# Optimization experiments

Measured on AMD Instinct MI355X. Metric: run time of the kernel, lower is better.

## Reference

```python
import jax, jax.numpy as jnp
import numpy as np

B, T, D, H, O = 128, 1024, 256, 512, 128


def _uniform(key, shape, std):
    return jax.random.uniform(key, shape, jnp.float32, -std, std)


def setup_inputs() -> dict:
    key = jax.random.key(0)
    ks = jax.random.split(key, 12)
    std = 1.0 / np.sqrt(H)
    return {
        "x": jax.random.normal(ks[0], (B, T, D), jnp.float32),
        "EC_in": jax.random.normal(ks[1], (B, T, D), jnp.float32),
        "Wx": _uniform(ks[2], (4 * H, D), std),   # x2h weight
        "bx": _uniform(ks[3], (4 * H,), std),
        "Wh": _uniform(ks[4], (4 * H, H), std),   # h2h weight
        "bh": _uniform(ks[5], (4 * H,), std),
        "Wec": _uniform(ks[6], (H, D), std),      # EC weight (dead code in original)
        "bec": _uniform(ks[7], (H,), std),
        "Wfc": _uniform(ks[8], (O, H), std),      # final fc weight
        "bfc": _uniform(ks[9], (O,), std),
    }


def _lstm_forward(x, EC_in, Wx, bx, Wh, bh, Wec, bec, Wfc, bfc):
    # Precompute input projections for all timesteps: [B,T,4H] -> [T,B,4H]
    xg = jnp.einsum("btd,gd->tbg", x, Wx) + bx + bh
    # NOTE: original computes self.EC(EC_in) per step but never uses it (dead code).

    def step(carry, xg_t):
        h, c = carry
        gates = xg_t + h @ Wh.T  # [B, 4H]
        i, f, g, o = jnp.split(gates, 4, axis=1)
        i = jax.nn.sigmoid(i)
        f = jax.nn.sigmoid(f)
        g = jnp.tanh(g)
        o = jax.nn.sigmoid(o)
        c = c * f + i * g
        h = o * jnp.tanh(c)
        return (h, c), None

    h0 = jnp.zeros((x.shape[0], Wh.shape[1]), x.dtype)
    (hT, cT), _ = jax.lax.scan(step, (h0, h0), xg)
    out = hT @ Wfc.T + bfc
    return hT, out


def reference(x, EC_in, Wx, bx, Wh, bh, Wec, bec, Wfc, bfc):
    return _lstm_forward(x, EC_in, Wx, bx, Wh, bh, Wec, bec, Wfc, bfc)
```

## Files before the change

### kernel.cpp

```cpp
#include <hip/hip_runtime.h>

typedef __bf16 bf16;
typedef __bf16 bf16x4 __attribute__((ext_vector_type(4)));
typedef __bf16 bf16x8 __attribute__((ext_vector_type(8)));
typedef float f32x4 __attribute__((ext_vector_type(4)));
typedef unsigned int u32;
typedef unsigned long long u64;

#define T_STEPS 1024
#define BATCH 128
#define DIM 256
#define HID 512
#define NB 128
#define NGRP 8
#define GB 16
#define FLAGS_BYTES 16384

__device__ __forceinline__ f32x4 mfma_bf16(bf16x8 a, bf16x8 b, f32x4 c) {
  return __builtin_amdgcn_mfma_f32_16x16x32_bf16(a, b, c, 0, 0, 0);
}
__device__ __forceinline__ float fast_sigmoid(float v) {
  return __builtin_amdgcn_rcpf(1.f + __expf(-v));
}
__device__ __forceinline__ float fast_tanh(float v) {
  return 2.f * __builtin_amdgcn_rcpf(1.f + __expf(-2.f * v)) - 1.f;
}
__device__ __forceinline__ bf16x8 cvt8(const float* p) {
  float4 a = *(const float4*)p;
  float4 b = *(const float4*)(p + 4);
  bf16x8 r;
  r[0] = (bf16)a.x; r[1] = (bf16)a.y; r[2] = (bf16)a.z; r[3] = (bf16)a.w;
  r[4] = (bf16)b.x; r[5] = (bf16)b.y; r[6] = (bf16)b.z; r[7] = (bf16)b.w;
  return r;
}
__device__ __forceinline__ bf16x8 cvt8v(float4 a, float4 b) {
  bf16x8 r;
  r[0] = (bf16)a.x; r[1] = (bf16)a.y; r[2] = (bf16)a.z; r[3] = (bf16)a.w;
  r[4] = (bf16)b.x; r[5] = (bf16)b.y; r[6] = (bf16)b.z; r[7] = (bf16)b.w;
  return r;
}
__device__ __forceinline__ u32 pack_bf16x2(float a, float b) {
  unsigned short lo = __builtin_bit_cast(unsigned short, (bf16)a);
  unsigned short hi = __builtin_bit_cast(unsigned short, (bf16)b);
  return (u32)lo | ((u32)hi << 16);
}
__device__ __forceinline__ bf16x8 combine(u64 lo, u64 hi) {
  bf16x4 l4 = __builtin_bit_cast(bf16x4, lo);
  bf16x4 h4 = __builtin_bit_cast(bf16x4, hi);
  bf16x8 r;
  r[0] = l4[0]; r[1] = l4[1]; r[2] = l4[2]; r[3] = l4[3];
  r[4] = h4[0]; r[5] = h4[1]; r[6] = h4[2]; r[7] = h4[3];
  return r;
}
__device__ __forceinline__ u64 ld_agent(const u64* p) {
  return __hip_atomic_load(p, __ATOMIC_RELAXED, __HIP_MEMORY_SCOPE_AGENT);
}

__device__ __forceinline__ void wait_all128(const u32* flags, int lane, u32 target) {
  const u32* p0 = flags + (size_t)lane * 16;
  const u32* p1 = flags + (size_t)(64 + lane) * 16;
  u32 a = __hip_atomic_load(p0, __ATOMIC_RELAXED, __HIP_MEMORY_SCOPE_AGENT);
  u32 b = __hip_atomic_load(p1, __ATOMIC_RELAXED, __HIP_MEMORY_SCOPE_AGENT);
  while (!__all((a >= target) && (b >= target))) {
    __builtin_amdgcn_s_sleep(1);
    a = __hip_atomic_load(p0, __ATOMIC_RELAXED, __HIP_MEMORY_SCOPE_AGENT);
    b = __hip_atomic_load(p1, __ATOMIC_RELAXED, __HIP_MEMORY_SCOPE_AGENT);
  }
}

__global__ __launch_bounds__(256, 1) void lstm_persist(
    const float* __restrict__ x, const float* __restrict__ Wx,
    const float* __restrict__ bx, const float* __restrict__ Wh,
    const float* __restrict__ bh, const float* __restrict__ Wfc,
    const float* __restrict__ bfc, float* __restrict__ out,
    u32* flags, bf16* hbuf) {
  const int tid = threadIdx.x;
  const int bid = blockIdx.x;
  const int wave = tid >> 6;
  const int lane = tid & 63;
  const int n = lane & 15;
  const int quad = lane >> 4;
  const int sub = n & 3;
  const int bg = bid & 7;
  const int cg = bid >> 3;
  const int mbase = bg * GB;

  __shared__ bf16 lds_h[16][520];

  const int R0 = (n >> 2) * HID + cg * 32 + wave * 8 + sub;
  const int R1 = R0 + 4;
  const float bias0 = bx[R0] + bh[R0];
  const float bias1 = bx[R1] + bh[R1];
  const f32x4 bv0 = {bias0, bias0, bias0, bias0};
  const f32x4 bv1 = {bias1, bias1, bias1, bias1};

  bf16x8 whf0[16], whf1[16];
#pragma unroll
  for (int k = 0; k < 16; ++k) {
    whf0[k] = cvt8(Wh + (size_t)R0 * HID + quad * 8 + k * 32);
    whf1[k] = cvt8(Wh + (size_t)R1 * HID + quad * 8 + k * 32);
  }
  bf16x8 wxf0[8], wxf1[8];
#pragma unroll
  for (int k = 0; k < 8; ++k) {
    wxf0[k] = cvt8(Wx + (size_t)R0 * DIM + quad * 8 + k * 32);
    wxf1[k] = cvt8(Wx + (size_t)R1 * DIM + quad * 8 + k * 32);
  }

  float cst[2][4];
#pragma unroll
  for (int a = 0; a < 2; ++a)
#pragma unroll
    for (int r = 0; r < 4; ++r) cst[a][r] = 0.f;

  const int qb = lane & 48;
  const int srcf = qb | (4 + sub);
  const int srcg = qb | (8 + sub);
  const int srco = qb | (12 + sub);

  const int grow = tid & 15;
  const int gchunk = tid >> 4;
  const u32* prodflag = flags + (size_t)(((gchunk << 3) | bg) * 16);

  const float* xrow = x + (size_t)(mbase + n) * 1024 * DIM + quad * 8;
  float4 xa[8], xb[8];
#pragma unroll
  for (int k = 0; k < 8; ++k) {
    xa[k] = *(const float4*)(xrow + k * 32);
    xb[k] = *(const float4*)(xrow + k * 32 + 4);
  }

  __syncthreads();

  for (int t = 0; t < T_STEPS; ++t) {
    const bf16* hrd = hbuf + (t & 1) * (BATCH * HID);
    bf16* hwr = hbuf + ((t + 1) & 1) * (BATCH * HID);

    f32x4 acc0 = bv0, acc1 = bv1;

#pragma unroll
    for (int k = 0; k < 8; ++k) {
      bf16x8 A = cvt8v(xa[k], xb[k]);
      acc0 = mfma_bf16(A, wxf0[k], acc0);
      acc1 = mfma_bf16(A, wxf1[k], acc1);
    }

    {
      const int tp = (t + 1 < T_STEPS) ? t + 1 : t;
      const float* xp = xrow + (size_t)tp * DIM;
#pragma unroll
      for (int k = 0; k < 8; ++k) {
        xa[k] = *(const float4*)(xp + k * 32);
        xb[k] = *(const float4*)(xp + k * 32 + 4);
      }
    }

    {
      const u64* src = (const u64*)hrd + (size_t)(mbase + grow) * (HID / 4) + gchunk * 8;
      u64 hv[8];
      bool done = false;
      while (true) {
        if (!done) {
          u32 f = __hip_atomic_load(prodflag, __ATOMIC_RELAXED, __HIP_MEMORY_SCOPE_AGENT);
          if (f >= (u32)t) {
#pragma unroll
            for (int j = 0; j < 8; ++j) hv[j] = ld_agent(src + j);
            done = true;
          }
        }
        if (__all(done)) break;
        __builtin_amdgcn_s_sleep(1);
      }
      u64* dst = (u64*)(&lds_h[grow][gchunk * 32]);
#pragma unroll
      for (int j = 0; j < 8; ++j) dst[j] = hv[j];
    }
    __syncthreads();

#pragma unroll
    for (int k = 0; k < 16; ++k) {
      bf16x8 A = *(const bf16x8*)(&lds_h[n][quad * 8 + k * 32]);
      acc0 = mfma_bf16(A, whf0[k], acc0);
      acc1 = mfma_bf16(A, whf1[k], acc1);
    }

    f32x4 accs[2] = {acc0, acc1};
#pragma unroll
    for (int nt = 0; nt < 2; ++nt) {
#pragma unroll
      for (int r = 0; r < 4; ++r) {
        float v = accs[nt][r];
        float s = fast_sigmoid(v);
        float th = fast_tanh(v);
        float pv = (n >= 8 && n < 12) ? th : s;
        float fv = __shfl(pv, srcf, 64);
        float gv = __shfl(pv, srcg, 64);
        float ov = __shfl(pv, srco, 64);
        float cn = cst[nt][r] * fv + pv * gv;
        float hn = ov * fast_tanh(cn);
        cst[nt][r] = cn;
        float h1 = __shfl(hn, qb | 1, 64);
        float h2 = __shfl(hn, qb | 2, 64);
        float h3 = __shfl(hn, qb | 3, 64);
        if (n == 0) {
          int m = mbase + quad * 4 + r;
          int c0 = cg * 32 + wave * 8 + nt * 4;
          u64 pk = (u64)pack_bf16x2(hn, h1) | ((u64)pack_bf16x2(h2, h3) << 32);
          __hip_atomic_store((u64*)(hwr + (size_t)m * HID + c0), pk,
                             __ATOMIC_RELAXED, __HIP_MEMORY_SCOPE_AGENT);
          if (t == T_STEPS - 1) {
            float4 o4 = {hn, h1, h2, h3};
            *(float4*)(out + (size_t)m * HID + c0) = o4;
          }
        }
      }
    }

    __syncthreads();
    if (tid == 0) {
      __hip_atomic_store(flags + (size_t)bid * 16, (u32)(t + 1),
                         __ATOMIC_RELAXED, __HIP_MEMORY_SCOPE_AGENT);
    }
  }

  if (bid < 8) {
    wait_all128(flags, lane, (u32)T_STEPS);
    float* out2 = out + BATCH * HID;
    int col = bid * 16 + n;
    float bcv = bfc[col];
#pragma unroll
    for (int mt = 0; mt < 2; ++mt) {
      int mb = wave * 32 + mt * 16;
      f32x4 a4 = {bcv, bcv, bcv, bcv};
      const u64* ar = (const u64*)hbuf + ((mb + n) * HID) / 4 + quad * 2;
      const float* br = Wfc + col * HID + quad * 8;
#pragma unroll
      for (int k = 0; k < HID; k += 32) {
        bf16x8 A = combine(ld_agent(ar + k / 4), ld_agent(ar + k / 4 + 1));
        bf16x8 B = cvt8(br + k);
        a4 = mfma_bf16(A, B, a4);
      }
#pragma unroll
      for (int r = 0; r < 4; ++r) {
        out2[(mb + quad * 4 + r) * 128 + col] = a4[r];
      }
    }
  }
}

extern "C" void kernel_launch(void* const* d_in, const int* in_sizes, int n_in,
                              void* d_out, int out_size, void* d_ws, size_t ws_size,
                              hipStream_t stream) {
  (void)in_sizes; (void)n_in; (void)out_size; (void)ws_size;
  const float* x   = (const float*)d_in[0];
  const float* Wx  = (const float*)d_in[2];
  const float* bx  = (const float*)d_in[3];
  const float* Wh  = (const float*)d_in[4];
  const float* bh  = (const float*)d_in[5];
  const float* Wfc = (const float*)d_in[8];
  const float* bfc = (const float*)d_in[9];
  float* out = (float*)d_out;
  u32* flags = (u32*)d_ws;
  bf16* hbuf = (bf16*)((char*)d_ws + FLAGS_BYTES);

  hipMemsetAsync(d_ws, 0, FLAGS_BYTES + 2 * BATCH * HID * sizeof(bf16), stream);
  lstm_persist<<<dim3(NB), dim3(256), 0, stream>>>(x, Wx, bx, Wh, bh, Wfc, bfc,
                                                   out, flags, hbuf);
}
```

Measured before the change: 6.007 ms.

## Replace per-block flags with sequence-tagged hidden-state words for inter-block sync

Each hidden value is now stored as a 32-bit word holding the bf16 value and a 16-bit step tag, so consumers poll the data itself instead of a producer flag followed by a separate load. This removes the per-step __syncthreads and flag store, and the flag-then-data round trip. The trade-off is double the hidden-state traffic and more validation work per read. The register prefetch of the next timestep's x is also dropped in favour of direct loads each step, which may expose x load latency on the critical path.

```diff
diff --git a/kernel.cpp b/kernel.cpp
--- a/kernel.cpp
+++ b/kernel.cpp
@@ -1,7 +1,6 @@
 #include <hip/hip_runtime.h>
 
 typedef __bf16 bf16;
-typedef __bf16 bf16x4 __attribute__((ext_vector_type(4)));
 typedef __bf16 bf16x8 __attribute__((ext_vector_type(8)));
 typedef float f32x4 __attribute__((ext_vector_type(4)));
 typedef unsigned int u32;
@@ -12,9 +11,7 @@
 #define DIM 256
 #define HID 512
 #define NB 128
-#define NGRP 8
 #define GB 16
-#define FLAGS_BYTES 16384
 
 __device__ __forceinline__ f32x4 mfma_bf16(bf16x8 a, bf16x8 b, f32x4 c) {
   return __builtin_amdgcn_mfma_f32_16x16x32_bf16(a, b, c, 0, 0, 0);
@@ -33,39 +30,25 @@
   r[4] = (bf16)b.x; r[5] = (bf16)b.y; r[6] = (bf16)b.z; r[7] = (bf16)b.w;
   return r;
 }
-__device__ __forceinline__ bf16x8 cvt8v(float4 a, float4 b) {
-  bf16x8 r;
-  r[0] = (bf16)a.x; r[1] = (bf16)a.y; r[2] = (bf16)a.z; r[3] = (bf16)a.w;
-  r[4] = (bf16)b.x; r[5] = (bf16)b.y; r[6] = (bf16)b.z; r[7] = (bf16)b.w;
-  return r;
-}
-__device__ __forceinline__ u32 pack_bf16x2(float a, float b) {
-  unsigned short lo = __builtin_bit_cast(unsigned short, (bf16)a);
-  unsigned short hi = __builtin_bit_cast(unsigned short, (bf16)b);
-  return (u32)lo | ((u32)hi << 16);
-}
-__device__ __forceinline__ bf16x8 combine(u64 lo, u64 hi) {
-  bf16x4 l4 = __builtin_bit_cast(bf16x4, lo);
-  bf16x4 h4 = __builtin_bit_cast(bf16x4, hi);
-  bf16x8 r;
-  r[0] = l4[0]; r[1] = l4[1]; r[2] = l4[2]; r[3] = l4[3];
-  r[4] = h4[0]; r[5] = h4[1]; r[6] = h4[2]; r[7] = h4[3];
-  return r;
-}
 __device__ __forceinline__ u64 ld_agent(const u64* p) {
   return __hip_atomic_load(p, __ATOMIC_RELAXED, __HIP_MEMORY_SCOPE_AGENT);
 }
-
-__device__ __forceinline__ void wait_all128(const u32* flags, int lane, u32 target) {
-  const u32* p0 = flags + (size_t)lane * 16;
-  const u32* p1 = flags + (size_t)(64 + lane) * 16;
-  u32 a = __hip_atomic_load(p0, __ATOMIC_RELAXED, __HIP_MEMORY_SCOPE_AGENT);
-  u32 b = __hip_atomic_load(p1, __ATOMIC_RELAXED, __HIP_MEMORY_SCOPE_AGENT);
-  while (!__all((a >= target) && (b >= target))) {
-    __builtin_amdgcn_s_sleep(1);
-    a = __hip_atomic_load(p0, __ATOMIC_RELAXED, __HIP_MEMORY_SCOPE_AGENT);
-    b = __hip_atomic_load(p1, __ATOMIC_RELAXED, __HIP_MEMORY_SCOPE_AGENT);
-  }
+__device__ __forceinline__ void st_agent(u64* p, u64 v) {
+  __hip_atomic_store(p, v, __ATOMIC_RELAXED, __HIP_MEMORY_SCOPE_AGENT);
+}
+__device__ __forceinline__ u32 pack_hs(float h, u32 seq) {
+  return (u32)__builtin_bit_cast(unsigned short, (bf16)h) | (seq << 16);
+}
+__device__ __forceinline__ bf16 bits16(u64 v) {
+  return __builtin_bit_cast(bf16, (unsigned short)(v & 0xffffu));
+}
+__device__ __forceinline__ bf16x8 seq8(u64 a, u64 b, u64 c, u64 d) {
+  bf16x8 r;
+  r[0] = bits16(a); r[1] = bits16(a >> 32);
+  r[2] = bits16(b); r[3] = bits16(b >> 32);
+  r[4] = bits16(c); r[5] = bits16(c >> 32);
+  r[6] = bits16(d); r[7] = bits16(d >> 32);
+  return r;
 }
 
 __global__ __launch_bounds__(256, 1) void lstm_persist(
@@ -73,7 +56,7 @@
     const float* __restrict__ bx, const float* __restrict__ Wh,
     const float* __restrict__ bh, const float* __restrict__ Wfc,
     const float* __restrict__ bfc, float* __restrict__ out,
-    u32* flags, bf16* hbuf) {
+    u32* hw) {
   const int tid = threadIdx.x;
   const int bid = blockIdx.x;
   const int wave = tid >> 6;
@@ -120,60 +103,44 @@
 
   const int grow = tid & 15;
   const int gchunk = tid >> 4;
-  const u32* prodflag = flags + (size_t)(((gchunk << 3) | bg) * 16);
-
-  const float* xrow = x + (size_t)(mbase + n) * 1024 * DIM + quad * 8;
-  float4 xa[8], xb[8];
-#pragma unroll
-  for (int k = 0; k < 8; ++k) {
-    xa[k] = *(const float4*)(xrow + k * 32);
-    xb[k] = *(const float4*)(xrow + k * 32 + 4);
-  }
-
-  __syncthreads();
 
   for (int t = 0; t < T_STEPS; ++t) {
-    const bf16* hrd = hbuf + (t & 1) * (BATCH * HID);
-    bf16* hwr = hbuf + ((t + 1) & 1) * (BATCH * HID);
+    u32* slot_rd = hw + (size_t)(t & 1) * (BATCH * HID);
+    u32* slot_wr = hw + (size_t)((t + 1) & 1) * (BATCH * HID);
 
     f32x4 acc0 = bv0, acc1 = bv1;
 
+    const float* x0p = x + (size_t)((mbase + n) * 1024 + t) * DIM + quad * 8;
 #pragma unroll
     for (int k = 0; k < 8; ++k) {
-      bf16x8 A = cvt8v(xa[k], xb[k]);
+      bf16x8 A = cvt8(x0p + k * 32);
       acc0 = mfma_bf16(A, wxf0[k], acc0);
       acc1 = mfma_bf16(A, wxf1[k], acc1);
     }
 
     {
-      const int tp = (t + 1 < T_STEPS) ? t + 1 : t;
-      const float* xp = xrow + (size_t)tp * DIM;
-#pragma unroll
-      for (int k = 0; k < 8; ++k) {
-        xa[k] = *(const float4*)(xp + k * 32);
-        xb[k] = *(const float4*)(xp + k * 32 + 4);
-      }
-    }
-
-    {
-      const u64* src = (const u64*)hrd + (size_t)(mbase + grow) * (HID / 4) + gchunk * 8;
-      u64 hv[8];
+      const u64* src = (const u64*)(slot_rd + (size_t)(mbase + grow) * HID + gchunk * 32);
       bool done = false;
       while (true) {
         if (!done) {
-          u32 f = __hip_atomic_load(prodflag, __ATOMIC_RELAXED, __HIP_MEMORY_SCOPE_AGENT);
-          if (f >= (u32)t) {
-#pragma unroll
-            for (int j = 0; j < 8; ++j) hv[j] = ld_agent(src + j);
+          u64 hv[16];
+#pragma unroll
+          for (int j = 0; j < 16; ++j) hv[j] = ld_agent(src + j);
+          bool v = true;
+#pragma unroll
+          for (int j = 0; j < 16; ++j) v &= (((hv[j] >> 16) & 0xffffu) == (u32)t);
+          if (v) {
+            u32* dst = (u32*)(&lds_h[grow][gchunk * 32]);
+#pragma unroll
+            for (int j = 0; j < 16; ++j) {
+              dst[j] = (u32)(hv[j] & 0xffffu) | ((u32)((hv[j] >> 32) & 0xffffu) << 16);
+            }
             done = true;
           }
         }
         if (__all(done)) break;
         __builtin_amdgcn_s_sleep(1);
       }
-      u64* dst = (u64*)(&lds_h[grow][gchunk * 32]);
-#pragma unroll
-      for (int j = 0; j < 8; ++j) dst[j] = hv[j];
     }
     __syncthreads();
 
@@ -205,9 +172,12 @@
         if (n == 0) {
           int m = mbase + quad * 4 + r;
           int c0 = cg * 32 + wave * 8 + nt * 4;
-          u64 pk = (u64)pack_bf16x2(hn, h1) | ((u64)pack_bf16x2(h2, h3) << 32);
-          __hip_atomic_store((u64*)(hwr + (size_t)m * HID + c0), pk,
-                             __ATOMIC_RELAXED, __HIP_MEMORY_SCOPE_AGENT);
+          u32 seq = (u32)(t + 1);
+          u64 lo = (u64)pack_hs(hn, seq) | ((u64)pack_hs(h1, seq) << 32);
+          u64 hi = (u64)pack_hs(h2, seq) | ((u64)pack_hs(h3, seq) << 32);
+          u64* hp = (u64*)(slot_wr + (size_t)m * HID + c0);
+          st_agent(hp + 0, lo);
+          st_agent(hp + 1, hi);
           if (t == T_STEPS - 1) {
             float4 o4 = {hn, h1, h2, h3};
             *(float4*)(out + (size_t)m * HID + c0) = o4;
@@ -215,16 +185,26 @@
         }
       }
     }
-
+  }
+
+  if (bid < 8) {
+    {
+      const u64* ps = (const u64*)hw + (size_t)tid * 128;
+      bool done = false;
+      while (true) {
+        if (!done) {
+          bool v = true;
+          for (int j = 0; j < 128; ++j) {
+            u64 e = ld_agent(ps + j);
+            v &= (((e >> 16) & 0xffffu) == (u32)T_STEPS);
+          }
+          if (v) done = true;
+        }
+        if (__all(done)) break;
+        __builtin_amdgcn_s_sleep(1);
+      }
+    }
     __syncthreads();
-    if (tid == 0) {
-      __hip_atomic_store(flags + (size_t)bid * 16, (u32)(t + 1),
-                         __ATOMIC_RELAXED, __HIP_MEMORY_SCOPE_AGENT);
-    }
-  }
-
-  if (bid < 8) {
-    wait_all128(flags, lane, (u32)T_STEPS);
     float* out2 = out + BATCH * HID;
     int col = bid * 16 + n;
     float bcv = bfc[col];
@@ -232,12 +212,13 @@
     for (int mt = 0; mt < 2; ++mt) {
       int mb = wave * 32 + mt * 16;
       f32x4 a4 = {bcv, bcv, bcv, bcv};
-      const u64* ar = (const u64*)hbuf + ((mb + n) * HID) / 4 + quad * 2;
+      const u64* ar = (const u64*)hw + (size_t)(mb + n) * (HID / 2) + quad * 4;
       const float* br = Wfc + col * HID + quad * 8;
 #pragma unroll
-      for (int k = 0; k < HID; k += 32) {
-        bf16x8 A = combine(ld_agent(ar + k / 4), ld_agent(ar + k / 4 + 1));
-        bf16x8 B = cvt8(br + k);
+      for (int k = 0; k < 16; ++k) {
+        const u64* p = ar + k * 16;
+        bf16x8 A = seq8(ld_agent(p), ld_agent(p + 1), ld_agent(p + 2), ld_agent(p + 3));
+        bf16x8 B = cvt8(br + k * 32);
         a4 = mfma_bf16(A, B, a4);
       }
 #pragma unroll
@@ -260,10 +241,9 @@
   const float* Wfc = (const float*)d_in[8];
   const float* bfc = (const float*)d_in[9];
   float* out = (float*)d_out;
-  u32* flags = (u32*)d_ws;
-  bf16* hbuf = (bf16*)((char*)d_ws + FLAGS_BYTES);
-
-  hipMemsetAsync(d_ws, 0, FLAGS_BYTES + 2 * BATCH * HID * sizeof(bf16), stream);
+  u32* hw = (u32*)d_ws;
+
+  hipMemsetAsync(d_ws, 0, (size_t)2 * BATCH * HID * sizeof(u32), stream);
   lstm_persist<<<dim3(NB), dim3(256), 0, stream>>>(x, Wx, bx, Wh, bh, Wfc, bfc,
-                                                   out, flags, hbuf);
-}
+                                                   out, hw);
+}
```

Result: slower. 7.564 ms (+25.9%).
